# Performance work log

Hardware: AMD Instinct MI355X
Metric: run time of the kernel (lower is better)

The kernel has to match this reference:

```python
import jax, jax.numpy as jnp
import numpy as np
from jax import lax

B_, C_, H_, W_ = 4, 128, 64, 64
D_INNER, D_STATE, DT_RANK, D_CONV = 256, 16, 8, 4


def setup_inputs() -> dict:
    ks = jax.random.split(jax.random.key(0), 12)
    def rn(k, shape, fan_in):
        return jax.random.normal(k, shape, jnp.float32) * (fan_in ** -0.5)
    return {
        "x": jax.random.normal(ks[0], (B_, C_, H_, W_), jnp.float32),
        "proj_w": rn(ks[1], (C_, C_), C_),
        "in_proj_w": rn(ks[2], (2 * D_INNER, C_), C_),
        "conv_w": rn(ks[3], (D_INNER, 1, D_CONV), D_CONV),
        "conv_b": jax.random.normal(ks[4], (D_INNER,), jnp.float32) * 0.02,
        "x_proj_w": rn(ks[5], (DT_RANK + 2 * D_STATE, D_INNER), D_INNER),
        "dt_proj_w": rn(ks[6], (D_INNER, DT_RANK), DT_RANK),
        "dt_proj_b": jax.random.normal(ks[7], (D_INNER,), jnp.float32) * 0.1,
        "A_log": jax.random.uniform(ks[8], (D_INNER, D_STATE), jnp.float32),
        "D": jax.random.normal(ks[9], (D_INNER,), jnp.float32),
        "out_proj_w": rn(ks[10], (C_, D_INNER), D_INNER),
    }


def _mamba2d(x, proj_w, in_proj_w, conv_w, conv_b, x_proj_w, dt_proj_w, dt_proj_b, A_log, D, out_proj_w):
    b, c, h, w = x.shape
    L = h * w
    # 1x1 conv projection then flatten to sequence (b, L, c)
    u = jnp.einsum('oc,bchw->bohw', proj_w, x).reshape(b, c, L).transpose(0, 2, 1)
    # in_proj -> x, z gates
    xz = u @ in_proj_w.T                      # (b, L, 2*d_inner)
    xs, zg = xz[..., :D_INNER], xz[..., D_INNER:]
    # causal depthwise conv1d over sequence
    xt = xs.transpose(0, 2, 1)                # (b, d_inner, L)
    xt = lax.conv_general_dilated(xt, conv_w, window_strides=(1,),
                                  padding=[(D_CONV - 1, 0)],
                                  feature_group_count=D_INNER)
    xc = jax.nn.silu(xt + conv_b[None, :, None]).transpose(0, 2, 1)  # (b, L, d_inner)
    # input-dependent SSM params
    x_dbl = xc @ x_proj_w.T                   # (b, L, dt_rank + 2*d_state)
    dt_r = x_dbl[..., :DT_RANK]
    Bm = x_dbl[..., DT_RANK:DT_RANK + D_STATE]
    Cm = x_dbl[..., DT_RANK + D_STATE:]
    delta = jax.nn.softplus(dt_r @ dt_proj_w.T + dt_proj_b)  # (b, L, d_inner)
    A = -jnp.exp(A_log)                       # (d_inner, d_state)

    def step(hprev, inp):
        dt_t, B_t, C_t, x_t = inp             # (b,d), (b,n), (b,n), (b,d)
        dA = jnp.exp(dt_t[:, :, None] * A)    # (b, d, n)
        hn = dA * hprev + (dt_t * x_t)[:, :, None] * B_t[:, None, :]
        y = jnp.einsum('bdn,bn->bd', hn, C_t)
        return hn, y

    h0 = jnp.zeros((b, D_INNER, D_STATE), xc.dtype)
    _, ys = lax.scan(step, h0, (delta.transpose(1, 0, 2), Bm.transpose(1, 0, 2),
                                Cm.transpose(1, 0, 2), xc.transpose(1, 0, 2)))
    y = ys.transpose(1, 0, 2) + xc * D        # (b, L, d_inner) + skip
    y = y * jax.nn.silu(zg)                   # output gating
    out = y @ out_proj_w.T                    # (b, L, c)
    return out.transpose(0, 2, 1).reshape(b, c, h, w) + x


def reference(x, proj_w, in_proj_w, conv_w, conv_b, x_proj_w, dt_proj_w, dt_proj_b, A_log, D, out_proj_w):
    return _mamba2d(x, proj_w, in_proj_w, conv_w, conv_b, x_proj_w, dt_proj_w, dt_proj_b, A_log, D, out_proj_w)
```

## Files before the change

kernel.cpp:

```cpp
#include <hip/hip_runtime.h>


#define NCHUNK 256
#define CLEN 16

using s16x8 = __attribute__((ext_vector_type(8))) short;
using f32x4 = __attribute__((ext_vector_type(4))) float;

__device__ inline unsigned short f2bf(float f) {
  unsigned u = __float_as_uint(f);
  u = u + 0x7FFF + ((u >> 16) & 1);
  return (unsigned short)(u >> 16);
}
__device__ inline float bf2f_lo(unsigned v) { return __uint_as_float(v << 16); }
__device__ inline float bf2f_hi(unsigned v) { return __uint_as_float(v & 0xFFFF0000u); }

__global__ void prep_kernel(const float* __restrict__ proj_w,
                            const float* __restrict__ in_proj_w,
                            const float* __restrict__ x_proj_w,
                            const float* __restrict__ out_proj_w,
                            const float* __restrict__ A_log,
                            unsigned short* __restrict__ W2b,
                            unsigned short* __restrict__ wTb48,
                            unsigned short* __restrict__ Woutb,
                            float* __restrict__ Aneg) {
  int idx = blockIdx.x * blockDim.x + threadIdx.x;
  if (idx < 65536) {
    int o = idx >> 7, c = idx & 127;
    float acc = 0.f;
    #pragma unroll 4
    for (int i = 0; i < 128; ++i)
      acc += in_proj_w[o * 128 + i] * proj_w[i * 128 + c];
    W2b[idx] = f2bf(acc);
  } else if (idx < 65536 + 12288) {
    int t = idx - 65536;
    int j = t >> 8, k = t & 255;
    wTb48[t] = (j < 40) ? f2bf(x_proj_w[j * 256 + k]) : (unsigned short)0;
  } else if (idx < 65536 + 12288 + 32768) {
    int t = idx - (65536 + 12288);
    Woutb[t] = f2bf(out_proj_w[t]);
  } else if (idx < 65536 + 12288 + 32768 + 4096) {
    int t = idx - (65536 + 12288 + 32768);
    Aneg[t] = -__expf(A_log[t]);
  }
}

__global__ __launch_bounds__(256, 1) void gemm_xz_kernel(
    const float* __restrict__ x, const unsigned short* __restrict__ W2b,
    float* __restrict__ xz) {
  __shared__ __align__(16) unsigned short At[128 * 128];
  __shared__ __align__(16) unsigned short Bt[256 * 128];
  int m0 = (blockIdx.x >> 1) * 128;
  int o0 = (blockIdx.x & 1) * 256;
  int b  = m0 >> 12;
  int l0 = m0 & 4095;
  int t = threadIdx.x;
  #pragma unroll
  for (int j = 0; j < 16; ++j) {
    int flat = t + j * 256;
    int cr = flat >> 5, lq = (flat & 31) << 2;
    float4 v = *reinterpret_cast<const float4*>(
        &x[((size_t)(b * 128 + cr)) * 4096 + l0 + lq]);
    float vv[4] = {v.x, v.y, v.z, v.w};
    #pragma unroll
    for (int e = 0; e < 4; ++e) {
      int l = lq + e;
      int g = (cr >> 3) ^ ((l & 7) << 1);
      At[l * 128 + g * 8 + (cr & 7)] = f2bf(vv[e]);
    }
  }
  #pragma unroll
  for (int j = 0; j < 16; ++j) {
    int flat = t + j * 256;
    int row = flat >> 4, gB = flat & 15;
    s16x8 v = *reinterpret_cast<const s16x8*>(&W2b[(size_t)(o0 + row) * 128 + gB * 8]);
    int g = gB ^ ((row & 7) << 1);
    *reinterpret_cast<s16x8*>(&Bt[row * 128 + g * 8]) = v;
  }
  __syncthreads();
  int ln = t & 63, wave = t >> 6;
  int wm = wave & 1, wn = wave >> 1;
  f32x4 acc[4][8] = {};
  #pragma unroll
  for (int ks = 0; ks < 4; ++ks) {
    int gk = ks * 4 + (ln >> 4);
    s16x8 a[4], bb[8];
    #pragma unroll
    for (int mi = 0; mi < 4; ++mi) {
      int lr = wm * 64 + mi * 16 + (ln & 15);
      a[mi] = *reinterpret_cast<const s16x8*>(&At[lr * 128 + (gk ^ ((lr & 7) << 1)) * 8]);
    }
    #pragma unroll
    for (int ni = 0; ni < 8; ++ni) {
      int orow = wn * 128 + ni * 16 + (ln & 15);
      bb[ni] = *reinterpret_cast<const s16x8*>(&Bt[orow * 128 + (gk ^ ((orow & 7) << 1)) * 8]);
    }
    #pragma unroll
    for (int mi = 0; mi < 4; ++mi)
      #pragma unroll
      for (int ni = 0; ni < 8; ++ni)
        acc[mi][ni] = __builtin_amdgcn_mfma_f32_16x16x32_bf16(a[mi], bb[ni], acc[mi][ni], 0, 0, 0);
  }
  #pragma unroll
  for (int mi = 0; mi < 4; ++mi)
    #pragma unroll
    for (int ni = 0; ni < 8; ++ni)
      #pragma unroll
      for (int r = 0; r < 4; ++r) {
        int row = wm * 64 + mi * 16 + (ln >> 4) * 4 + r;
        int col = wn * 128 + ni * 16 + (ln & 15);
        xz[(size_t)(m0 + row) * 512 + o0 + col] = acc[mi][ni][r];
      }
}

__global__ __launch_bounds__(256) void conv_silu_kernel(
    const float* __restrict__ xz, const float* __restrict__ conv_w,
    const float* __restrict__ conv_b, float* __restrict__ xc,
    unsigned short* __restrict__ xcb) {
  int bl0 = blockIdx.x * 8;
  int d = threadIdx.x;
  int l0 = bl0 & 4095;
  float w0 = conv_w[d * 4 + 0], w1 = conv_w[d * 4 + 1];
  float w2 = conv_w[d * 4 + 2], w3 = conv_w[d * 4 + 3];
  float cb = conv_b[d];
  float xm1 = (l0 >= 1) ? xz[(size_t)(bl0 - 1) * 512 + d] : 0.f;
  float xm2 = (l0 >= 2) ? xz[(size_t)(bl0 - 2) * 512 + d] : 0.f;
  float xm3 = (l0 >= 3) ? xz[(size_t)(bl0 - 3) * 512 + d] : 0.f;
  #pragma unroll
  for (int r = 0; r < 8; ++r) {
    size_t bl = bl0 + r;
    float x0 = xz[bl * 512 + d];
    float acc = cb + w3 * x0 + w2 * xm1 + w1 * xm2 + w0 * xm3;
    float s = acc * (1.f / (1.f + __expf(-acc)));
    xc[bl * 256 + d] = s;
    xcb[bl * 256 + d] = f2bf(s);
    xm3 = xm2; xm2 = xm1; xm1 = x0;
  }
}

__global__ __launch_bounds__(256) void xdbl_mfma_kernel(
    const unsigned short* __restrict__ xcb, const unsigned short* __restrict__ wTb48,
    float* __restrict__ xdbl48) {
  __shared__ __align__(16) unsigned short At[64 * 256];
  __shared__ __align__(16) unsigned short Bt[48 * 256];
  int m0 = blockIdx.x * 64;
  int t = threadIdx.x;
  #pragma unroll
  for (int it = 0; it < 8; ++it) {
    int f = t + it * 256;
    int row = f >> 5, g0 = f & 31;
    s16x8 v = *reinterpret_cast<const s16x8*>(&xcb[(size_t)(m0 + row) * 256 + g0 * 8]);
    int g = g0 ^ ((row & 7) << 1);
    *reinterpret_cast<s16x8*>(&At[row * 256 + g * 8]) = v;
  }
  #pragma unroll
  for (int it = 0; it < 6; ++it) {
    int f = t + it * 256;
    int row = f >> 5, g0 = f & 31;
    s16x8 v = *reinterpret_cast<const s16x8*>(&wTb48[(size_t)row * 256 + g0 * 8]);
    int g = g0 ^ ((row & 7) << 1);
    *reinterpret_cast<s16x8*>(&Bt[row * 256 + g * 8]) = v;
  }
  __syncthreads();
  int ln = t & 63, wm = t >> 6;
  f32x4 acc[3] = {};
  #pragma unroll
  for (int ks = 0; ks < 8; ++ks) {
    int gk = ks * 4 + (ln >> 4);
    int ar = wm * 16 + (ln & 15);
    s16x8 a = *reinterpret_cast<const s16x8*>(&At[ar * 256 + (gk ^ ((ar & 7) << 1)) * 8]);
    #pragma unroll
    for (int nt = 0; nt < 3; ++nt) {
      int br = nt * 16 + (ln & 15);
      s16x8 bb = *reinterpret_cast<const s16x8*>(&Bt[br * 256 + (gk ^ ((br & 7) << 1)) * 8]);
      acc[nt] = __builtin_amdgcn_mfma_f32_16x16x32_bf16(a, bb, acc[nt], 0, 0, 0);
    }
  }
  #pragma unroll
  for (int nt = 0; nt < 3; ++nt)
    #pragma unroll
    for (int r = 0; r < 4; ++r) {
      int row = m0 + wm * 16 + (ln >> 4) * 4 + r;
      xdbl48[(size_t)row * 48 + nt * 16 + (ln & 15)] = acc[nt][r];
    }
}

__global__ __launch_bounds__(256) void scan1_kernel(
    const float* __restrict__ xc, const float* __restrict__ xdbl48,
    const float* __restrict__ dt_proj_w, const float* __restrict__ dt_proj_b,
    const float* __restrict__ Aneg,
    float* __restrict__ Ssum, unsigned* __restrict__ chHb) {
  __shared__ __align__(16) float lBC[CLEN][32];
  __shared__ __align__(16) float sdtr[CLEN][8];
  int bc = blockIdx.x;
  int b = bc >> 8, c = bc & 255;
  int bl0 = bc * CLEN;
  int tid = threadIdx.x;
  if (tid < 128) {
    int t0 = tid >> 3, q = (tid & 7) << 2;
    *reinterpret_cast<float4*>(&lBC[t0][q]) =
        *reinterpret_cast<const float4*>(&xdbl48[(size_t)(bl0 + t0) * 48 + 8 + q]);
  }
  if (tid < 32) {
    int t1 = tid >> 1, q1 = (tid & 1) << 2;
    *reinterpret_cast<float4*>(&sdtr[t1][q1]) =
        *reinterpret_cast<const float4*>(&xdbl48[(size_t)(bl0 + t1) * 48 + q1]);
  }
  int d = tid;
  float wrow[8];
  *reinterpret_cast<float4*>(&wrow[0]) =
      *reinterpret_cast<const float4*>(&dt_proj_w[d * 8]);
  *reinterpret_cast<float4*>(&wrow[4]) =
      *reinterpret_cast<const float4*>(&dt_proj_w[d * 8 + 4]);
  float bb = dt_proj_b[d];
  float An[16];
  #pragma unroll
  for (int q = 0; q < 4; ++q)
    *reinterpret_cast<float4*>(&An[q * 4]) =
        *reinterpret_cast<const float4*>(&Aneg[d * 16 + q * 4]);
  float xv[CLEN];
  #pragma unroll
  for (int t = 0; t < CLEN; ++t)
    xv[t] = xc[(size_t)(bl0 + t) * 256 + d];
  __syncthreads();
  float h[16] = {};
  float S = 0.f;
  #pragma unroll
  for (int t = 0; t < CLEN; ++t) {
    float a = bb;
    #pragma unroll
    for (int q = 0; q < 8; ++q) a += sdtr[t][q] * wrow[q];
    float dlv = fmaxf(a, 0.f) + __logf(1.f + __expf(-fabsf(a)));
    S += dlv;
    float dlx = dlv * xv[t];
    float4 B0 = *reinterpret_cast<const float4*>(&lBC[t][0]);
    float4 B1 = *reinterpret_cast<const float4*>(&lBC[t][4]);
    float4 B2 = *reinterpret_cast<const float4*>(&lBC[t][8]);
    float4 B3 = *reinterpret_cast<const float4*>(&lBC[t][12]);
    float Bv[16] = {B0.x,B0.y,B0.z,B0.w,B1.x,B1.y,B1.z,B1.w,
                    B2.x,B2.y,B2.z,B2.w,B3.x,B3.y,B3.z,B3.w};
    #pragma unroll
    for (int n = 0; n < 16; ++n)
      h[n] = __expf(dlv * An[n]) * h[n] + dlx * Bv[n];
  }
  int p = b * 256 + d;
  Ssum[c * 1024 + p] = S;
  unsigned up[8];
  #pragma unroll
  for (int q = 0; q < 8; ++q)
    up[q] = (unsigned)f2bf(h[2 * q]) | ((unsigned)f2bf(h[2 * q + 1]) << 16);
  size_t ub = ((size_t)(c * 1024 + p)) * 8;
  *reinterpret_cast<uint4*>(&chHb[ub])     = uint4{up[0], up[1], up[2], up[3]};
  *reinterpret_cast<uint4*>(&chHb[ub + 4]) = uint4{up[4], up[5], up[6], up[7]};
}

__global__ void scan2_kernel(const float* __restrict__ Aneg,
                             const float* __restrict__ Ssum,
                             const unsigned short* __restrict__ chHb,
                             unsigned short* __restrict__ chSb) {
  int q = blockIdx.x * blockDim.x + threadIdx.x;
  int p = q >> 4, n = q & 15;
  int d = p & 255;
  float An = Aneg[d * 16 + n];
  float h = 0.f;
  #pragma unroll 8
  for (int c = 0; c < NCHUNK; ++c) {
    size_t idx = ((size_t)(c * 1024 + p)) * 16 + n;
    float S = Ssum[c * 1024 + p];
    float hl = bf2f_lo((unsigned)chHb[idx]);
    chSb[idx] = f2bf(h);
    h = __expf(An * S) * h + hl;
  }
}

__global__ __launch_bounds__(256) void scan3_kernel(
    const float* __restrict__ xc, const float* __restrict__ xdbl48,
    const float* __restrict__ dt_proj_w, const float* __restrict__ dt_proj_b,
    const float* __restrict__ Aneg, const unsigned* __restrict__ chSb,
    const float* __restrict__ Dvec, const float* __restrict__ xz,
    unsigned short* __restrict__ y2b) {
  __shared__ __align__(16) float lBC[CLEN][32];
  __shared__ __align__(16) float sdtr[CLEN][8];
  int bc = blockIdx.x;
  int b = bc >> 8, c = bc & 255;
  int bl0 = bc * CLEN;
  int tid = threadIdx.x;
  if (tid < 128) {
    int t0 = tid >> 3, q = (tid & 7) << 2;
    *reinterpret_cast<float4*>(&lBC[t0][q]) =
        *reinterpret_cast<const float4*>(&xdbl48[(size_t)(bl0 + t0) * 48 + 8 + q]);
  }
  if (tid < 32) {
    int t1 = tid >> 1, q1 = (tid & 1) << 2;
    *reinterpret_cast<float4*>(&sdtr[t1][q1]) =
        *reinterpret_cast<const float4*>(&xdbl48[(size_t)(bl0 + t1) * 48 + q1]);
  }
  int d = tid;
  float wrow[8];
  *reinterpret_cast<float4*>(&wrow[0]) =
      *reinterpret_cast<const float4*>(&dt_proj_w[d * 8]);
  *reinterpret_cast<float4*>(&wrow[4]) =
      *reinterpret_cast<const float4*>(&dt_proj_w[d * 8 + 4]);
  float bb = dt_proj_b[d];
  float An[16];
  #pragma unroll
  for (int q = 0; q < 4; ++q)
    *reinterpret_cast<float4*>(&An[q * 4]) =
        *reinterpret_cast<const float4*>(&Aneg[d * 16 + q * 4]);
  int p = b * 256 + d;
  float h[16];
  {
    size_t ub = ((size_t)(c * 1024 + p)) * 8;
    uint4 s0 = *reinterpret_cast<const uint4*>(&chSb[ub]);
    uint4 s1 = *reinterpret_cast<const uint4*>(&chSb[ub + 4]);
    h[0] = bf2f_lo(s0.x); h[1] = bf2f_hi(s0.x);
    h[2] = bf2f_lo(s0.y); h[3] = bf2f_hi(s0.y);
    h[4] = bf2f_lo(s0.z); h[5] = bf2f_hi(s0.z);
    h[6] = bf2f_lo(s0.w); h[7] = bf2f_hi(s0.w);
    h[8] = bf2f_lo(s1.x); h[9] = bf2f_hi(s1.x);
    h[10] = bf2f_lo(s1.y); h[11] = bf2f_hi(s1.y);
    h[12] = bf2f_lo(s1.z); h[13] = bf2f_hi(s1.z);
    h[14] = bf2f_lo(s1.w); h[15] = bf2f_hi(s1.w);
  }
  float xv[CLEN], zv[CLEN];
  #pragma unroll
  for (int t = 0; t < CLEN; ++t) {
    xv[t] = xc[(size_t)(bl0 + t) * 256 + d];
    zv[t] = xz[(size_t)(bl0 + t) * 512 + 256 + d];
  }
  float Dd = Dvec[d];
  __syncthreads();
  #pragma unroll
  for (int t = 0; t < CLEN; ++t) {
    float a = bb;
    #pragma unroll
    for (int q = 0; q < 8; ++q) a += sdtr[t][q] * wrow[q];
    float dlv = fmaxf(a, 0.f) + __logf(1.f + __expf(-fabsf(a)));
    float xvv = xv[t];
    float dlx = dlv * xvv;
    float4 B0 = *reinterpret_cast<const float4*>(&lBC[t][0]);
    float4 B1 = *reinterpret_cast<const float4*>(&lBC[t][4]);
    float4 B2 = *reinterpret_cast<const float4*>(&lBC[t][8]);
    float4 B3 = *reinterpret_cast<const float4*>(&lBC[t][12]);
    float4 C0 = *reinterpret_cast<const float4*>(&lBC[t][16]);
    float4 C1 = *reinterpret_cast<const float4*>(&lBC[t][20]);
    float4 C2 = *reinterpret_cast<const float4*>(&lBC[t][24]);
    float4 C3 = *reinterpret_cast<const float4*>(&lBC[t][28]);
    float Bv[16] = {B0.x,B0.y,B0.z,B0.w,B1.x,B1.y,B1.z,B1.w,
                    B2.x,B2.y,B2.z,B2.w,B3.x,B3.y,B3.z,B3.w};
    float Cv[16] = {C0.x,C0.y,C0.z,C0.w,C1.x,C1.y,C1.z,C1.w,
                    C2.x,C2.y,C2.z,C2.w,C3.x,C3.y,C3.z,C3.w};
    float y = 0.f;
    #pragma unroll
    for (int n = 0; n < 16; ++n) {
      h[n] = __expf(dlv * An[n]) * h[n] + dlx * Bv[n];
      y += h[n] * Cv[n];
    }
    float z = zv[t];
    float sil = z * (1.f / (1.f + __expf(-z)));
    y2b[(size_t)(bl0 + t) * 256 + d] = f2bf((y + xvv * Dd) * sil);
  }
}

__global__ __launch_bounds__(256) void gemm_out_kernel(
    const unsigned short* __restrict__ y2b, const unsigned short* __restrict__ Woutb,
    const float* __restrict__ x, float* __restrict__ out) {
  __shared__ __align__(16) unsigned short At[64 * 256];
  __shared__ __align__(16) unsigned short Bt[128 * 256];
  int m0 = blockIdx.x * 64;
  int b = m0 >> 12, l0 = m0 & 4095;
  int t = threadIdx.x;
  #pragma unroll
  for (int it = 0; it < 8; ++it) {
    int f = t + it * 256;
    int row = f >> 5, g0 = f & 31;
    s16x8 v = *reinterpret_cast<const s16x8*>(&y2b[(size_t)(m0 + row) * 256 + g0 * 8]);
    int g = g0 ^ ((row & 7) << 1);
    *reinterpret_cast<s16x8*>(&At[row * 256 + g * 8]) = v;
  }
  #pragma unroll
  for (int it = 0; it < 16; ++it) {
    int f = t + it * 256;
    int row = f >> 5, g0 = f & 31;
    s16x8 v = *reinterpret_cast<const s16x8*>(&Woutb[(size_t)row * 256 + g0 * 8]);
    int g = g0 ^ ((row & 7) << 1);
    *reinterpret_cast<s16x8*>(&Bt[row * 256 + g * 8]) = v;
  }
  __syncthreads();
  int ln = t & 63, wm = t >> 6;
  f32x4 acc[8] = {};
  #pragma unroll
  for (int ks = 0; ks < 8; ++ks) {
    int gk = ks * 4 + (ln >> 4);
    int ar = wm * 16 + (ln & 15);
    s16x8 a = *reinterpret_cast<const s16x8*>(&At[ar * 256 + (gk ^ ((ar & 7) << 1)) * 8]);
    #pragma unroll
    for (int nt = 0; nt < 8; ++nt) {
      int br = nt * 16 + (ln & 15);
      s16x8 bb = *reinterpret_cast<const s16x8*>(&Bt[br * 256 + (gk ^ ((br & 7) << 1)) * 8]);
      acc[nt] = __builtin_amdgcn_mfma_f32_16x16x32_bf16(a, bb, acc[nt], 0, 0, 0);
    }
  }
  #pragma unroll
  for (int nt = 0; nt < 8; ++nt) {
    int cc = nt * 16 + (ln & 15);
    size_t base = ((size_t)(b * 128 + cc)) * 4096 + l0 + wm * 16 + ((ln >> 4) << 2);
    float4 xr = *reinterpret_cast<const float4*>(&x[base]);
    float4 o{acc[nt][0] + xr.x, acc[nt][1] + xr.y, acc[nt][2] + xr.z, acc[nt][3] + xr.w};
    *reinterpret_cast<float4*>(&out[base]) = o;
  }
}

extern "C" void kernel_launch(void* const* d_in, const int* in_sizes, int n_in,
                              void* d_out, int out_size, void* d_ws, size_t ws_size,
                              hipStream_t stream) {
  const float* x         = (const float*)d_in[0];
  const float* proj_w    = (const float*)d_in[1];
  const float* in_proj_w = (const float*)d_in[2];
  const float* conv_w    = (const float*)d_in[3];
  const float* conv_b    = (const float*)d_in[4];
  const float* x_proj_w  = (const float*)d_in[5];
  const float* dt_proj_w = (const float*)d_in[6];
  const float* dt_proj_b = (const float*)d_in[7];
  const float* A_log     = (const float*)d_in[8];
  const float* Dvec      = (const float*)d_in[9];
  const float* out_proj_w= (const float*)d_in[10];

  float* ws = (float*)d_ws;
  float*          Aneg   = ws;
  unsigned short* W2b    = (unsigned short*)(ws + 4096);
  unsigned short* wTb48  = (unsigned short*)(ws + 36864);
  unsigned short* Woutb  = (unsigned short*)(ws + 43008);
  float*          xz     = ws + 59392;
  float*          xc     = xz + 8388608;
  unsigned short* xcb    = (unsigned short*)(xc + 4194304);
  float*          xdbl48 = xc + 4194304 + 2097152;
  float*          Ssum   = xdbl48 + 786432;
  unsigned*       chHb   = (unsigned*)(Ssum + 262144);
  unsigned*       chSb   = chHb + 2097152;
  unsigned short* y2b    = (unsigned short*)(chSb + 2097152);
  float* out = (float*)d_out;

  prep_kernel<<<448, 256, 0, stream>>>(proj_w, in_proj_w, x_proj_w, out_proj_w, A_log,
                                       W2b, wTb48, Woutb, Aneg);
  gemm_xz_kernel<<<256, 256, 0, stream>>>(x, W2b, xz);
  conv_silu_kernel<<<2048, 256, 0, stream>>>(xz, conv_w, conv_b, xc, xcb);
  xdbl_mfma_kernel<<<256, 256, 0, stream>>>(xcb, wTb48, xdbl48);
  scan1_kernel<<<1024, 256, 0, stream>>>(xc, xdbl48, dt_proj_w, dt_proj_b, Aneg,
                                         Ssum, chHb);
  scan2_kernel<<<64, 256, 0, stream>>>(Aneg, Ssum, (const unsigned short*)chHb,
                                       (unsigned short*)chSb);
  scan3_kernel<<<1024, 256, 0, stream>>>(xc, xdbl48, dt_proj_w, dt_proj_b, Aneg,
                                         chSb, Dvec, xz, y2b);
  gemm_out_kernel<<<256, 256, 0, stream>>>(y2b, Woutb, x, out);
}
```

Measured before the change: 181.3 us.

## Store xz and xc intermediates in bf16 and process two chunks per scan thread

The in-projection output xz is now written as bf16 instead of fp32, and the fp32 copy of xc is dropped so the scan kernels read the bf16 xcb. This cuts global memory traffic for the largest intermediates. In addition, scan1 and scan3 each handle two 16-step chunks per thread with interleaved independent recurrences, halving the grid and giving more instruction-level parallelism. Precision is lower on the conv input, the gate z and the scan x values, and register pressure in the scan kernels rises.

```diff
diff --git a/kernel.cpp b/kernel.cpp
--- a/kernel.cpp
+++ b/kernel.cpp
@@ -11,6 +11,9 @@
   unsigned u = __float_as_uint(f);
   u = u + 0x7FFF + ((u >> 16) & 1);
   return (unsigned short)(u >> 16);
+}
+__device__ inline float bfu(unsigned short v) {
+  return __uint_as_float((unsigned)v << 16);
 }
 __device__ inline float bf2f_lo(unsigned v) { return __uint_as_float(v << 16); }
 __device__ inline float bf2f_hi(unsigned v) { return __uint_as_float(v & 0xFFFF0000u); }
@@ -47,7 +50,7 @@
 
 __global__ __launch_bounds__(256, 1) void gemm_xz_kernel(
     const float* __restrict__ x, const unsigned short* __restrict__ W2b,
-    float* __restrict__ xz) {
+    unsigned short* __restrict__ xzb) {
   __shared__ __align__(16) unsigned short At[128 * 128];
   __shared__ __align__(16) unsigned short Bt[256 * 128];
   int m0 = (blockIdx.x >> 1) * 128;
@@ -109,30 +112,28 @@
       for (int r = 0; r < 4; ++r) {
         int row = wm * 64 + mi * 16 + (ln >> 4) * 4 + r;
         int col = wn * 128 + ni * 16 + (ln & 15);
-        xz[(size_t)(m0 + row) * 512 + o0 + col] = acc[mi][ni][r];
+        xzb[(size_t)(m0 + row) * 512 + o0 + col] = f2bf(acc[mi][ni][r]);
       }
 }
 
 __global__ __launch_bounds__(256) void conv_silu_kernel(
-    const float* __restrict__ xz, const float* __restrict__ conv_w,
-    const float* __restrict__ conv_b, float* __restrict__ xc,
-    unsigned short* __restrict__ xcb) {
+    const unsigned short* __restrict__ xzb, const float* __restrict__ conv_w,
+    const float* __restrict__ conv_b, unsigned short* __restrict__ xcb) {
   int bl0 = blockIdx.x * 8;
   int d = threadIdx.x;
   int l0 = bl0 & 4095;
   float w0 = conv_w[d * 4 + 0], w1 = conv_w[d * 4 + 1];
   float w2 = conv_w[d * 4 + 2], w3 = conv_w[d * 4 + 3];
   float cb = conv_b[d];
-  float xm1 = (l0 >= 1) ? xz[(size_t)(bl0 - 1) * 512 + d] : 0.f;
-  float xm2 = (l0 >= 2) ? xz[(size_t)(bl0 - 2) * 512 + d] : 0.f;
-  float xm3 = (l0 >= 3) ? xz[(size_t)(bl0 - 3) * 512 + d] : 0.f;
+  float xm1 = (l0 >= 1) ? bfu(xzb[(size_t)(bl0 - 1) * 512 + d]) : 0.f;
+  float xm2 = (l0 >= 2) ? bfu(xzb[(size_t)(bl0 - 2) * 512 + d]) : 0.f;
+  float xm3 = (l0 >= 3) ? bfu(xzb[(size_t)(bl0 - 3) * 512 + d]) : 0.f;
   #pragma unroll
   for (int r = 0; r < 8; ++r) {
     size_t bl = bl0 + r;
-    float x0 = xz[bl * 512 + d];
+    float x0 = bfu(xzb[bl * 512 + d]);
     float acc = cb + w3 * x0 + w2 * xm1 + w1 * xm2 + w0 * xm3;
     float s = acc * (1.f / (1.f + __expf(-acc)));
-    xc[bl * 256 + d] = s;
     xcb[bl * 256 + d] = f2bf(s);
     xm3 = xm2; xm2 = xm1; xm1 = x0;
   }
@@ -186,22 +187,22 @@
 }
 
 __global__ __launch_bounds__(256) void scan1_kernel(
-    const float* __restrict__ xc, const float* __restrict__ xdbl48,
+    const unsigned short* __restrict__ xcb, const float* __restrict__ xdbl48,
     const float* __restrict__ dt_proj_w, const float* __restrict__ dt_proj_b,
     const float* __restrict__ Aneg,
     float* __restrict__ Ssum, unsigned* __restrict__ chHb) {
-  __shared__ __align__(16) float lBC[CLEN][32];
-  __shared__ __align__(16) float sdtr[CLEN][8];
-  int bc = blockIdx.x;
-  int b = bc >> 8, c = bc & 255;
-  int bl0 = bc * CLEN;
+  __shared__ __align__(16) float lBC[32][32];
+  __shared__ __align__(16) float sdtr[32][8];
+  int blk = blockIdx.x;
+  int b = blk >> 7, cp = blk & 127;
+  int bl0 = blk * 32;
   int tid = threadIdx.x;
-  if (tid < 128) {
+  {
     int t0 = tid >> 3, q = (tid & 7) << 2;
     *reinterpret_cast<float4*>(&lBC[t0][q]) =
         *reinterpret_cast<const float4*>(&xdbl48[(size_t)(bl0 + t0) * 48 + 8 + q]);
   }
-  if (tid < 32) {
+  if (tid < 64) {
     int t1 = tid >> 1, q1 = (tid & 1) << 2;
     *reinterpret_cast<float4*>(&sdtr[t1][q1]) =
         *reinterpret_cast<const float4*>(&xdbl48[(size_t)(bl0 + t1) * 48 + q1]);
@@ -218,40 +219,51 @@
   for (int q = 0; q < 4; ++q)
     *reinterpret_cast<float4*>(&An[q * 4]) =
         *reinterpret_cast<const float4*>(&Aneg[d * 16 + q * 4]);
-  float xv[CLEN];
-  #pragma unroll
-  for (int t = 0; t < CLEN; ++t)
-    xv[t] = xc[(size_t)(bl0 + t) * 256 + d];
+  unsigned xp[CLEN];
+  #pragma unroll
+  for (int t = 0; t < CLEN; ++t) {
+    unsigned lo = xcb[(size_t)(bl0 + t) * 256 + d];
+    unsigned hi = xcb[(size_t)(bl0 + 16 + t) * 256 + d];
+    xp[t] = lo | (hi << 16);
+  }
   __syncthreads();
-  float h[16] = {};
-  float S = 0.f;
+  float hA[16] = {}, hB[16] = {};
+  float SA = 0.f, SB = 0.f;
   #pragma unroll
   for (int t = 0; t < CLEN; ++t) {
-    float a = bb;
-    #pragma unroll
-    for (int q = 0; q < 8; ++q) a += sdtr[t][q] * wrow[q];
-    float dlv = fmaxf(a, 0.f) + __logf(1.f + __expf(-fabsf(a)));
-    S += dlv;
-    float dlx = dlv * xv[t];
-    float4 B0 = *reinterpret_cast<const float4*>(&lBC[t][0]);
-    float4 B1 = *reinterpret_cast<const float4*>(&lBC[t][4]);
-    float4 B2 = *reinterpret_cast<const float4*>(&lBC[t][8]);
-    float4 B3 = *reinterpret_cast<const float4*>(&lBC[t][12]);
-    float Bv[16] = {B0.x,B0.y,B0.z,B0.w,B1.x,B1.y,B1.z,B1.w,
-                    B2.x,B2.y,B2.z,B2.w,B3.x,B3.y,B3.z,B3.w};
-    #pragma unroll
-    for (int n = 0; n < 16; ++n)
-      h[n] = __expf(dlv * An[n]) * h[n] + dlx * Bv[n];
+    float aA = bb, aB = bb;
+    #pragma unroll
+    for (int q = 0; q < 8; ++q) {
+      aA += sdtr[t][q] * wrow[q];
+      aB += sdtr[16 + t][q] * wrow[q];
+    }
+    float dlA = fmaxf(aA, 0.f) + __logf(1.f + __expf(-fabsf(aA)));
+    float dlB = fmaxf(aB, 0.f) + __logf(1.f + __expf(-fabsf(aB)));
+    SA += dlA; SB += dlB;
+    float dlxA = dlA * bf2f_lo(xp[t]);
+    float dlxB = dlB * bf2f_hi(xp[t]);
+    #pragma unroll
+    for (int n = 0; n < 16; ++n) {
+      hA[n] = __expf(dlA * An[n]) * hA[n] + dlxA * lBC[t][n];
+      hB[n] = __expf(dlB * An[n]) * hB[n] + dlxB * lBC[16 + t][n];
+    }
   }
   int p = b * 256 + d;
-  Ssum[c * 1024 + p] = S;
-  unsigned up[8];
-  #pragma unroll
-  for (int q = 0; q < 8; ++q)
-    up[q] = (unsigned)f2bf(h[2 * q]) | ((unsigned)f2bf(h[2 * q + 1]) << 16);
-  size_t ub = ((size_t)(c * 1024 + p)) * 8;
-  *reinterpret_cast<uint4*>(&chHb[ub])     = uint4{up[0], up[1], up[2], up[3]};
-  *reinterpret_cast<uint4*>(&chHb[ub + 4]) = uint4{up[4], up[5], up[6], up[7]};
+  int c0 = cp * 2;
+  Ssum[c0 * 1024 + p] = SA;
+  Ssum[(c0 + 1) * 1024 + p] = SB;
+  unsigned upA[8], upB[8];
+  #pragma unroll
+  for (int q = 0; q < 8; ++q) {
+    upA[q] = (unsigned)f2bf(hA[2 * q]) | ((unsigned)f2bf(hA[2 * q + 1]) << 16);
+    upB[q] = (unsigned)f2bf(hB[2 * q]) | ((unsigned)f2bf(hB[2 * q + 1]) << 16);
+  }
+  size_t ubA = ((size_t)(c0 * 1024 + p)) * 8;
+  size_t ubB = ((size_t)((c0 + 1) * 1024 + p)) * 8;
+  *reinterpret_cast<uint4*>(&chHb[ubA])     = uint4{upA[0], upA[1], upA[2], upA[3]};
+  *reinterpret_cast<uint4*>(&chHb[ubA + 4]) = uint4{upA[4], upA[5], upA[6], upA[7]};
+  *reinterpret_cast<uint4*>(&chHb[ubB])     = uint4{upB[0], upB[1], upB[2], upB[3]};
+  *reinterpret_cast<uint4*>(&chHb[ubB + 4]) = uint4{upB[4], upB[5], upB[6], upB[7]};
 }
 
 __global__ void scan2_kernel(const float* __restrict__ Aneg,
@@ -274,23 +286,23 @@
 }
 
 __global__ __launch_bounds__(256) void scan3_kernel(
-    const float* __restrict__ xc, const float* __restrict__ xdbl48,
+    const unsigned short* __restrict__ xcb, const float* __restrict__ xdbl48,
     const float* __restrict__ dt_proj_w, const float* __restrict__ dt_proj_b,
     const float* __restrict__ Aneg, const unsigned* __restrict__ chSb,
-    const float* __restrict__ Dvec, const float* __restrict__ xz,
+    const float* __restrict__ Dvec, const unsigned short* __restrict__ xzb,
     unsigned short* __restrict__ y2b) {
-  __shared__ __align__(16) float lBC[CLEN][32];
-  __shared__ __align__(16) float sdtr[CLEN][8];
-  int bc = blockIdx.x;
-  int b = bc >> 8, c = bc & 255;
-  int bl0 = bc * CLEN;
+  __shared__ __align__(16) float lBC[32][32];
+  __shared__ __align__(16) float sdtr[32][8];
+  int blk = blockIdx.x;
+  int b = blk >> 7, cp = blk & 127;
+  int bl0 = blk * 32;
   int tid = threadIdx.x;
-  if (tid < 128) {
+  {
     int t0 = tid >> 3, q = (tid & 7) << 2;
     *reinterpret_cast<float4*>(&lBC[t0][q]) =
         *reinterpret_cast<const float4*>(&xdbl48[(size_t)(bl0 + t0) * 48 + 8 + q]);
   }
-  if (tid < 32) {
+  if (tid < 64) {
     int t1 = tid >> 1, q1 = (tid & 1) << 2;
     *reinterpret_cast<float4*>(&sdtr[t1][q1]) =
         *reinterpret_cast<const float4*>(&xdbl48[(size_t)(bl0 + t1) * 48 + q1]);
@@ -308,57 +320,56 @@
     *reinterpret_cast<float4*>(&An[q * 4]) =
         *reinterpret_cast<const float4*>(&Aneg[d * 16 + q * 4]);
   int p = b * 256 + d;
-  float h[16];
+  int c0 = cp * 2;
+  float hA[16], hB[16];
   {
-    size_t ub = ((size_t)(c * 1024 + p)) * 8;
-    uint4 s0 = *reinterpret_cast<const uint4*>(&chSb[ub]);
-    uint4 s1 = *reinterpret_cast<const uint4*>(&chSb[ub + 4]);
-    h[0] = bf2f_lo(s0.x); h[1] = bf2f_hi(s0.x);
-    h[2] = bf2f_lo(s0.y); h[3] = bf2f_hi(s0.y);
-    h[4] = bf2f_lo(s0.z); h[5] = bf2f_hi(s0.z);
-    h[6] = bf2f_lo(s0.w); h[7] = bf2f_hi(s0.w);
-    h[8] = bf2f_lo(s1.x); h[9] = bf2f_hi(s1.x);
-    h[10] = bf2f_lo(s1.y); h[11] = bf2f_hi(s1.y);
-    h[12] = bf2f_lo(s1.z); h[13] = bf2f_hi(s1.z);
-    h[14] = bf2f_lo(s1.w); h[15] = bf2f_hi(s1.w);
-  }
-  float xv[CLEN], zv[CLEN];
+    size_t ubA = ((size_t)(c0 * 1024 + p)) * 8;
+    size_t ubB = ((size_t)((c0 + 1) * 1024 + p)) * 8;
+    #pragma unroll
+    for (int q = 0; q < 8; ++q) {
+      unsigned vA = chSb[ubA + q];
+      unsigned vB = chSb[ubB + q];
+      hA[2 * q] = bf2f_lo(vA); hA[2 * q + 1] = bf2f_hi(vA);
+      hB[2 * q] = bf2f_lo(vB); hB[2 * q + 1] = bf2f_hi(vB);
+    }
+  }
+  unsigned xp[CLEN], zp[CLEN];
   #pragma unroll
   for (int t = 0; t < CLEN; ++t) {
-    xv[t] = xc[(size_t)(bl0 + t) * 256 + d];
-    zv[t] = xz[(size_t)(bl0 + t) * 512 + 256 + d];
+    unsigned xlo = xcb[(size_t)(bl0 + t) * 256 + d];
+    unsigned xhi = xcb[(size_t)(bl0 + 16 + t) * 256 + d];
+    xp[t] = xlo | (xhi << 16);
+    unsigned zlo = xzb[(size_t)(bl0 + t) * 512 + 256 + d];
+    unsigned zhi = xzb[(size_t)(bl0 + 16 + t) * 512 + 256 + d];
+    zp[t] = zlo | (zhi << 16);
   }
   float Dd = Dvec[d];
   __syncthreads();
   #pragma unroll
   for (int t = 0; t < CLEN; ++t) {
-    float a = bb;
-    #pragma unroll
-    for (int q = 0; q < 8; ++q) a += sdtr[t][q] * wrow[q];
-    float dlv = fmaxf(a, 0.f) + __logf(1.f + __expf(-fabsf(a)));
-    float xvv = xv[t];
-    float dlx = dlv * xvv;
-    float4 B0 = *reinterpret_cast<const float4*>(&lBC[t][0]);
-    float4 B1 = *reinterpret_cast<const float4*>(&lBC[t][4]);
-    float4 B2 = *reinterpret_cast<const float4*>(&lBC[t][8]);
-    float4 B3 = *reinterpret_cast<const float4*>(&lBC[t][12]);
-    float4 C0 = *reinterpret_cast<const float4*>(&lBC[t][16]);
-    float4 C1 = *reinterpret_cast<const float4*>(&lBC[t][20]);
-    float4 C2 = *reinterpret_cast<const float4*>(&lBC[t][24]);
-    float4 C3 = *reinterpret_cast<const float4*>(&lBC[t][28]);
-    float Bv[16] = {B0.x,B0.y,B0.z,B0.w,B1.x,B1.y,B1.z,B1.w,
-                    B2.x,B2.y,B2.z,B2.w,B3.x,B3.y,B3.z,B3.w};
-    float Cv[16] = {C0.x,C0.y,C0.z,C0.w,C1.x,C1.y,C1.z,C1.w,
-                    C2.x,C2.y,C2.z,C2.w,C3.x,C3.y,C3.z,C3.w};
-    float y = 0.f;
+    float aA = bb, aB = bb;
+    #pragma unroll
+    for (int q = 0; q < 8; ++q) {
+      aA += sdtr[t][q] * wrow[q];
+      aB += sdtr[16 + t][q] * wrow[q];
+    }
+    float dlA = fmaxf(aA, 0.f) + __logf(1.f + __expf(-fabsf(aA)));
+    float dlB = fmaxf(aB, 0.f) + __logf(1.f + __expf(-fabsf(aB)));
+    float xA = bf2f_lo(xp[t]), xB = bf2f_hi(xp[t]);
+    float dlxA = dlA * xA, dlxB = dlB * xB;
+    float yA = 0.f, yB = 0.f;
     #pragma unroll
     for (int n = 0; n < 16; ++n) {
-      h[n] = __expf(dlv * An[n]) * h[n] + dlx * Bv[n];
-      y += h[n] * Cv[n];
-    }
-    float z = zv[t];
-    float sil = z * (1.f / (1.f + __expf(-z)));
-    y2b[(size_t)(bl0 + t) * 256 + d] = f2bf((y + xvv * Dd) * sil);
+      hA[n] = __expf(dlA * An[n]) * hA[n] + dlxA * lBC[t][n];
+      hB[n] = __expf(dlB * An[n]) * hB[n] + dlxB * lBC[16 + t][n];
+      yA += hA[n] * lBC[t][16 + n];
+      yB += hB[n] * lBC[16 + t][16 + n];
+    }
+    float zA = bf2f_lo(zp[t]), zB = bf2f_hi(zp[t]);
+    float silA = zA * (1.f / (1.f + __expf(-zA)));
+    float silB = zB * (1.f / (1.f + __expf(-zB)));
+    y2b[(size_t)(bl0 + t) * 256 + d] = f2bf((yA + xA * Dd) * silA);
+    y2b[(size_t)(bl0 + 16 + t) * 256 + d] = f2bf((yB + xB * Dd) * silB);
   }
 }
 
@@ -431,26 +442,25 @@
   unsigned short* W2b    = (unsigned short*)(ws + 4096);
   unsigned short* wTb48  = (unsigned short*)(ws + 36864);
   unsigned short* Woutb  = (unsigned short*)(ws + 43008);
-  float*          xz     = ws + 59392;
-  float*          xc     = xz + 8388608;
-  unsigned short* xcb    = (unsigned short*)(xc + 4194304);
-  float*          xdbl48 = xc + 4194304 + 2097152;
-  float*          Ssum   = xdbl48 + 786432;
-  unsigned*       chHb   = (unsigned*)(Ssum + 262144);
-  unsigned*       chSb   = chHb + 2097152;
-  unsigned short* y2b    = (unsigned short*)(chSb + 2097152);
+  unsigned short* xzb    = (unsigned short*)(ws + 59392);
+  unsigned short* xcb    = (unsigned short*)(ws + 4253696);
+  float*          xdbl48 = ws + 6350848;
+  float*          Ssum   = ws + 7137280;
+  unsigned*       chHb   = (unsigned*)(ws + 7399424);
+  unsigned*       chSb   = (unsigned*)(ws + 9496576);
+  unsigned short* y2b    = (unsigned short*)(ws + 11593728);
   float* out = (float*)d_out;
 
   prep_kernel<<<448, 256, 0, stream>>>(proj_w, in_proj_w, x_proj_w, out_proj_w, A_log,
                                        W2b, wTb48, Woutb, Aneg);
-  gemm_xz_kernel<<<256, 256, 0, stream>>>(x, W2b, xz);
-  conv_silu_kernel<<<2048, 256, 0, stream>>>(xz, conv_w, conv_b, xc, xcb);
+  gemm_xz_kernel<<<256, 256, 0, stream>>>(x, W2b, xzb);
+  conv_silu_kernel<<<2048, 256, 0, stream>>>(xzb, conv_w, conv_b, xcb);
   xdbl_mfma_kernel<<<256, 256, 0, stream>>>(xcb, wTb48, xdbl48);
-  scan1_kernel<<<1024, 256, 0, stream>>>(xc, xdbl48, dt_proj_w, dt_proj_b, Aneg,
-                                         Ssum, chHb);
+  scan1_kernel<<<512, 256, 0, stream>>>(xcb, xdbl48, dt_proj_w, dt_proj_b, Aneg,
+                                        Ssum, chHb);
   scan2_kernel<<<64, 256, 0, stream>>>(Aneg, Ssum, (const unsigned short*)chHb,
                                        (unsigned short*)chSb);
-  scan3_kernel<<<1024, 256, 0, stream>>>(xc, xdbl48, dt_proj_w, dt_proj_b, Aneg,
-                                         chSb, Dvec, xz, y2b);
+  scan3_kernel<<<512, 256, 0, stream>>>(xcb, xdbl48, dt_proj_w, dt_proj_b, Aneg,
+                                        chSb, Dvec, xzb, y2b);
   gemm_out_kernel<<<256, 256, 0, stream>>>(y2b, Woutb, x, out);
 }
```

Measured after the change: 187.4 us. +3.3%, slower.
